# Performance work log

Hardware: AMD Instinct MI355X
Metric: run time of the kernel (lower is better)

The kernel has to match this reference:

```python
import jax, jax.numpy as jnp
import numpy as np

N = 65536   # nodes
E = 1048576 # edges
D_IN = 128
D_H = 64
D_OUT = 2


def setup_inputs() -> dict:
    key = jax.random.key(0)
    ks = jax.random.split(key, 16)
    inp = {
        "x": jax.random.normal(ks[0], (N, D_IN), dtype=jnp.float32),
        "edge_index": jax.random.randint(ks[1], (2, E), 0, N, dtype=jnp.int64),
        "edge_attr": jax.random.uniform(ks[2], (E,), dtype=jnp.float32),
        "W1": jax.random.normal(ks[3], (D_IN, D_H), dtype=jnp.float32) / np.sqrt(D_IN),
        "b1": jnp.zeros((D_H,), dtype=jnp.float32),
        "W2": jax.random.normal(ks[4], (D_H, D_H), dtype=jnp.float32) / np.sqrt(D_H),
        "b2": jnp.zeros((D_H,), dtype=jnp.float32),
        "W3": jax.random.normal(ks[5], (D_H, D_H), dtype=jnp.float32) / np.sqrt(D_H),
        "b3": jnp.zeros((D_H,), dtype=jnp.float32),
        "W4": jax.random.normal(ks[6], (D_H, D_H), dtype=jnp.float32) / np.sqrt(D_H),
        "b4": jnp.zeros((D_H,), dtype=jnp.float32),
        "W5": jax.random.normal(ks[7], (D_H, D_H), dtype=jnp.float32) / np.sqrt(D_H),
        "b5": jnp.zeros((D_H,), dtype=jnp.float32),
        "W8": jax.random.normal(ks[8], (D_H, D_OUT), dtype=jnp.float32) / np.sqrt(D_H),
        "b8": jnp.zeros((D_OUT,), dtype=jnp.float32),
    }
    return inp


def _gcn_layer(x, W, b, row, col, norm):
    # linear transform then degree-normalized scatter-add over edges
    h = x @ W                                              # [N, d_out]
    agg = jax.ops.segment_sum(norm[:, None] * h[row], col, num_segments=N)
    return agg + b


def reference(x, edge_index, edge_attr, W1, b1, W2, b2, W3, b3, W4, b4, W5, b5, W8, b8):
    # gcn_norm with self-loops (PyG GCNConv semantics), shared by all layers
    loop = jnp.arange(N, dtype=edge_index.dtype)
    row = jnp.concatenate([edge_index[0], loop])           # [E+N] sources
    col = jnp.concatenate([edge_index[1], loop])           # [E+N] targets
    ew = jnp.concatenate([edge_attr, jnp.ones((N,), dtype=edge_attr.dtype)])
    deg = jax.ops.segment_sum(ew, col, num_segments=N)     # weighted in-degree
    dinv = jnp.where(deg > 0, deg ** -0.5, 0.0)
    norm = dinv[row] * ew * dinv[col]                      # [E+N]

    h = jax.nn.relu(_gcn_layer(x, W1, b1, row, col, norm))
    h = jax.nn.relu(_gcn_layer(h, W2, b2, row, col, norm))
    # dropout p=0.2 is identity at inference
    h = jax.nn.relu(_gcn_layer(h, W3, b3, row, col, norm))
    h = jax.nn.relu(_gcn_layer(h, W4, b4, row, col, norm))
    h = jax.nn.relu(_gcn_layer(h, W5, b5, row, col, norm))
    return _gcn_layer(h, W8, b8, row, col, norm)           # [N, 2]
```

## Files before the change

### kernel.cpp

```cpp
#include <hip/hip_runtime.h>
#include <hip/hip_bf16.h>
#include <math.h>

#define NN 65536
#define NE 1048576
#define DEG_SCALE 33554432.0f

__device__ inline float4 f4fma(float s, float4 v, float4 a) {
    a.x = fmaf(s, v.x, a.x);
    a.y = fmaf(s, v.y, a.y);
    a.z = fmaf(s, v.z, a.z);
    a.w = fmaf(s, v.w, a.w);
    return a;
}

__device__ inline unsigned pack2bf(float a, float b) {
    __hip_bfloat16 ha = __float2bfloat16(a), hb = __float2bfloat16(b);
    return (unsigned)*reinterpret_cast<unsigned short*>(&ha) |
           ((unsigned)*reinterpret_cast<unsigned short*>(&hb) << 16);
}

__device__ inline void bfx8(uint4 v, float* f) {
    f[0] = __uint_as_float(v.x << 16);
    f[1] = __uint_as_float(v.x & 0xffff0000u);
    f[2] = __uint_as_float(v.y << 16);
    f[3] = __uint_as_float(v.y & 0xffff0000u);
    f[4] = __uint_as_float(v.z << 16);
    f[5] = __uint_as_float(v.z & 0xffff0000u);
    f[6] = __uint_as_float(v.w << 16);
    f[7] = __uint_as_float(v.w & 0xffff0000u);
}

template <int K>
__device__ void mm64_body_bf(const float* __restrict__ A, const float* __restrict__ W,
                             unsigned short* __restrict__ Cb, int node0, int tid) {
    __shared__ float As[64 * 68];
    __shared__ float Ws[64 * 64];
    const int tx = tid & 15;
    const int ty = tid >> 4;
    float4 acc[4];
#pragma unroll
    for (int m = 0; m < 4; ++m) acc[m] = make_float4(0.f, 0.f, 0.f, 0.f);

    for (int kc = 0; kc < K; kc += 64) {
#pragma unroll
        for (int p = 0; p < 4; ++p) {
            int idx = tid + p * 256;
            int r = idx >> 4, c4 = idx & 15;
            float4 v = *reinterpret_cast<const float4*>(A + (size_t)(node0 + r) * K + kc + c4 * 4);
            *reinterpret_cast<float4*>(&As[r * 68 + c4 * 4]) = v;
        }
#pragma unroll
        for (int p = 0; p < 4; ++p) {
            int idx = tid + p * 256;
            int r = idx >> 4, c4 = idx & 15;
            float4 v = *reinterpret_cast<const float4*>(W + (size_t)(kc + r) * 64 + c4 * 4);
            *reinterpret_cast<float4*>(&Ws[r * 64 + c4 * 4]) = v;
        }
        __syncthreads();
#pragma unroll 16
        for (int k = 0; k < 64; ++k) {
            float4 w = *reinterpret_cast<const float4*>(&Ws[k * 64 + tx * 4]);
            float a0 = As[(ty * 4 + 0) * 68 + k];
            float a1 = As[(ty * 4 + 1) * 68 + k];
            float a2 = As[(ty * 4 + 2) * 68 + k];
            float a3 = As[(ty * 4 + 3) * 68 + k];
            acc[0] = f4fma(a0, w, acc[0]);
            acc[1] = f4fma(a1, w, acc[1]);
            acc[2] = f4fma(a2, w, acc[2]);
            acc[3] = f4fma(a3, w, acc[3]);
        }
        __syncthreads();
    }
#pragma unroll
    for (int m = 0; m < 4; ++m) {
        uint2 pk;
        pk.x = pack2bf(acc[m].x, acc[m].y);
        pk.y = pack2bf(acc[m].z, acc[m].w);
        *reinterpret_cast<uint2*>(Cb + (size_t)(node0 + ty * 4 + m) * 64 + tx * 4) = pk;
    }
}


__global__ void __launch_bounds__(256) setup_mm(const int* __restrict__ col,
                                                const float* __restrict__ ew,
                                                unsigned long long* __restrict__ cntdeg,
                                                int* __restrict__ rank,
                                                const float* __restrict__ x,
                                                const float* __restrict__ W1,
                                                unsigned short* __restrict__ Tb) {
    const int bid = blockIdx.x;
    const int tid = threadIdx.x;
    if (bid % 5 == 0) {
        mm64_body_bf<128>(x, W1, Tb, (bid / 5) * 64, tid);
    } else {
        int e = (bid - bid / 5 - 1) * 256 + tid;
        if (e < NE) {
            int c = col[e];
            unsigned long long p =
                (1ull << 32) | (unsigned long long)__float2uint_rn(ew[e] * DEG_SCALE);
            unsigned long long old = atomicAdd(&cntdeg[c], p);
            rank[e] = (int)(old >> 32);
        }
    }
}

__global__ void __launch_bounds__(256) scan1(const unsigned long long* __restrict__ cntdeg,
                                             int* __restrict__ row_ptr,
                                             int* __restrict__ blocksum,
                                             float* __restrict__ dinv) {
    __shared__ int ls[256];
    const int t = threadIdx.x;
    const int i = blockIdx.x * 256 + t;
    unsigned long long v = cntdeg[i];
    const int c = (int)(v >> 32);
    float deg = (float)(unsigned)(v & 0xffffffffull) * (1.0f / DEG_SCALE) + 1.0f;
    dinv[i] = 1.0f / sqrtf(deg);
    ls[t] = c;
    __syncthreads();
#pragma unroll
    for (int off = 1; off < 256; off <<= 1) {
        int u = (t >= off) ? ls[t - off] : 0;
        __syncthreads();
        ls[t] += u;
        __syncthreads();
    }
    row_ptr[i] = ls[t] - c;
    if (t == 255) blocksum[blockIdx.x] = ls[255];
}

__global__ void __launch_bounds__(256) scan2(int* __restrict__ blocksum,
                                             int* __restrict__ blockbase,
                                             int* __restrict__ row_ptr) {
    __shared__ int ls[256];
    const int t = threadIdx.x;
    const int c = blocksum[t];
    ls[t] = c;
    __syncthreads();
#pragma unroll
    for (int off = 1; off < 256; off <<= 1) {
        int u = (t >= off) ? ls[t - off] : 0;
        __syncthreads();
        ls[t] += u;
        __syncthreads();
    }
    blockbase[t] = ls[t] - c;
    if (t == 255) row_ptr[NN] = ls[255];
}

__global__ void __launch_bounds__(256) scan3(int* __restrict__ row_ptr,
                                             const int* __restrict__ blockbase) {
    const int i = blockIdx.x * 256 + threadIdx.x;
    row_ptr[i] += blockbase[blockIdx.x];
}

__global__ void __launch_bounds__(256) fill_kernel(const int* __restrict__ row,
                                                   const int* __restrict__ col,
                                                   const float* __restrict__ ew,
                                                   const float* __restrict__ dinv,
                                                   const int* __restrict__ row_ptr,
                                                   const int* __restrict__ rank,
                                                   int2* __restrict__ epack) {
    int e = blockIdx.x * 256 + threadIdx.x;
    if (e < NE) {
        int c = col[e], r = row[e];
        int idx = row_ptr[c] + rank[e];
        int2 p;
        p.x = r;
        p.y = __float_as_int(dinv[r] * ew[e] * dinv[c]);
        epack[idx] = p;
    }
}


__device__ inline void gather_node(const uint4* __restrict__ T4,
                                   const float* __restrict__ bias,
                                   const float* __restrict__ dinv,
                                   const int* __restrict__ row_ptr,
                                   const int2* __restrict__ epack,
                                   int node, int l, float* acc) {
    const float dv = dinv[node];
    {
        float ts[8];
        bfx8(T4[(size_t)node * 8 + l], ts);
        float4 bA = *reinterpret_cast<const float4*>(bias + l * 8);
        float4 bB = *reinterpret_cast<const float4*>(bias + l * 8 + 4);
        acc[0] = bA.x + dv * dv * ts[0];
        acc[1] = bA.y + dv * dv * ts[1];
        acc[2] = bA.z + dv * dv * ts[2];
        acc[3] = bA.w + dv * dv * ts[3];
        acc[4] = bB.x + dv * dv * ts[4];
        acc[5] = bB.y + dv * dv * ts[5];
        acc[6] = bB.z + dv * dv * ts[6];
        acc[7] = bB.w + dv * dv * ts[7];
    }
    const int s = row_ptr[node];
    const int e = row_ptr[node + 1];
    for (int i0 = s; i0 < e; i0 += 8) {
        int2 p[8];
#pragma unroll
        for (int j = 0; j < 8; ++j) {
            int ii = i0 + j;
            p[j] = epack[ii < e ? ii : i0];
        }
        uint4 r[8];
        float n[8];
#pragma unroll
        for (int j = 0; j < 8; ++j) {
            n[j] = (i0 + j < e) ? __int_as_float(p[j].y) : 0.0f;
            r[j] = T4[(size_t)p[j].x * 8 + l];
        }
#pragma unroll
        for (int j = 0; j < 8; ++j) {
            float f[8];
            bfx8(r[j], f);
#pragma unroll
            for (int k = 0; k < 8; ++k) acc[k] = fmaf(n[j], f[k], acc[k]);
        }
    }
#pragma unroll
    for (int k = 0; k < 8; ++k) acc[k] = fmaxf(acc[k], 0.f);
}

__global__ void __launch_bounds__(256) gmm64(const unsigned short* __restrict__ Tb,
                                             const float* __restrict__ bias,
                                             const float* __restrict__ dinv,
                                             const int* __restrict__ row_ptr,
                                             const int2* __restrict__ epack,
                                             const float* __restrict__ W,
                                             unsigned short* __restrict__ Tbn) {
    __shared__ float As[32 * 68];
    __shared__ float Ws[64 * 64];
    const int tid = threadIdx.x;
    const int node0 = blockIdx.x * 32;

#pragma unroll
    for (int p = 0; p < 4; ++p) {
        int idx = tid + p * 256;
        int r = idx >> 4, c4 = idx & 15;
        *reinterpret_cast<float4*>(&Ws[r * 64 + c4 * 4]) =
            *reinterpret_cast<const float4*>(W + (size_t)r * 64 + c4 * 4);
    }

    const int l = tid & 7;
    const int slot = tid >> 3;
    float acc[8];
    gather_node(reinterpret_cast<const uint4*>(Tb), bias, dinv, row_ptr, epack,
                node0 + slot, l, acc);
    *reinterpret_cast<float4*>(&As[slot * 68 + l * 8]) =
        make_float4(acc[0], acc[1], acc[2], acc[3]);
    *reinterpret_cast<float4*>(&As[slot * 68 + l * 8 + 4]) =
        make_float4(acc[4], acc[5], acc[6], acc[7]);
    __syncthreads();

    const int tx = tid & 15;
    const int ty = tid >> 4;
    float4 c0 = make_float4(0.f, 0.f, 0.f, 0.f);
    float4 c1 = make_float4(0.f, 0.f, 0.f, 0.f);
#pragma unroll 16
    for (int k = 0; k < 64; ++k) {
        float4 w = *reinterpret_cast<const float4*>(&Ws[k * 64 + tx * 4]);
        float a0 = As[(ty * 2 + 0) * 68 + k];
        float a1 = As[(ty * 2 + 1) * 68 + k];
        c0 = f4fma(a0, w, c0);
        c1 = f4fma(a1, w, c1);
    }
    uint2 pk;
    pk.x = pack2bf(c0.x, c0.y);
    pk.y = pack2bf(c0.z, c0.w);
    *reinterpret_cast<uint2*>(Tbn + (size_t)(node0 + ty * 2 + 0) * 64 + tx * 4) = pk;
    pk.x = pack2bf(c1.x, c1.y);
    pk.y = pack2bf(c1.z, c1.w);
    *reinterpret_cast<uint2*>(Tbn + (size_t)(node0 + ty * 2 + 1) * 64 + tx * 4) = pk;
}

__global__ void __launch_bounds__(256) gmm2(const unsigned short* __restrict__ Tb,
                                            const float* __restrict__ bias,
                                            const float* __restrict__ dinv,
                                            const int* __restrict__ row_ptr,
                                            const int2* __restrict__ epack,
                                            const float* __restrict__ W8,
                                            float* __restrict__ T8) {
    __shared__ float As[32 * 68];
    const int tid = threadIdx.x;
    const int node0 = blockIdx.x * 32;
    const int l = tid & 7;
    const int slot = tid >> 3;
    float acc[8];
    gather_node(reinterpret_cast<const uint4*>(Tb), bias, dinv, row_ptr, epack,
                node0 + slot, l, acc);
    *reinterpret_cast<float4*>(&As[slot * 68 + l * 8]) =
        make_float4(acc[0], acc[1], acc[2], acc[3]);
    *reinterpret_cast<float4*>(&As[slot * 68 + l * 8 + 4]) =
        make_float4(acc[4], acc[5], acc[6], acc[7]);
    __syncthreads();
    if (tid < 64) {
        const int nd = tid >> 1, c = tid & 1;
        float s = 0.f;
#pragma unroll 16
        for (int k = 0; k < 64; ++k) s = fmaf(As[nd * 68 + k], W8[k * 2 + c], s);
        T8[(size_t)(node0 + nd) * 2 + c] = s;
    }
}

__global__ void __launch_bounds__(256) gather2(const float* __restrict__ T8,
                                               const float* __restrict__ b8,
                                               const float* __restrict__ dinv,
                                               const int* __restrict__ row_ptr,
                                               const int2* __restrict__ epack,
                                               float* __restrict__ out) {
    const int lane = threadIdx.x & 63;
    const int c = lane & 1;
    const int j = lane >> 1;
    const int node = blockIdx.x * 4 + (threadIdx.x >> 6);
    const int s = row_ptr[node];
    const int e = row_ptr[node + 1];
    float acc = 0.f;
    for (int i = s + j; i < e; i += 32) {
        int2 p = epack[i];
        acc += __int_as_float(p.y) * T8[(size_t)p.x * 2 + c];
    }
    acc += __shfl_xor(acc, 2);
    acc += __shfl_xor(acc, 4);
    acc += __shfl_xor(acc, 8);
    acc += __shfl_xor(acc, 16);
    acc += __shfl_xor(acc, 32);
    if (j == 0) {
        const float dv = dinv[node];
        out[(size_t)node * 2 + c] = b8[c] + dv * dv * T8[(size_t)node * 2 + c] + acc;
    }
}


extern "C" void kernel_launch(void* const* d_in, const int* in_sizes, int n_in,
                              void* d_out, int out_size, void* d_ws, size_t ws_size,
                              hipStream_t stream) {
    const float* x  = (const float*)d_in[0];
    const int*   ei = (const int*)d_in[1];
    const float* ea = (const float*)d_in[2];
    const float* W1 = (const float*)d_in[3];
    const float* b1 = (const float*)d_in[4];
    const float* W2 = (const float*)d_in[5];
    const float* b2 = (const float*)d_in[6];
    const float* W3 = (const float*)d_in[7];
    const float* b3 = (const float*)d_in[8];
    const float* W4 = (const float*)d_in[9];
    const float* b4 = (const float*)d_in[10];
    const float* W5 = (const float*)d_in[11];
    const float* b5 = (const float*)d_in[12];
    const float* W8 = (const float*)d_in[13];
    const float* b8 = (const float*)d_in[14];
    float* out = (float*)d_out;

    unsigned short* Tb1 = (unsigned short*)d_ws;
    unsigned short* Tb2 = Tb1 + (size_t)NN * 64;
    int*   rank   = (int*)Tb2;
    int2*  epack  = (int2*)(Tb2 + (size_t)NN * 64);
    unsigned long long* cntdeg = (unsigned long long*)(epack + NE);
    float* dinv   = (float*)(cntdeg + NN);
    int*   row_ptr= (int*)(dinv + NN);
    float* T8     = (float*)(row_ptr + NN + 1);
    int*   blocksum  = (int*)(T8 + (size_t)NN * 2);
    int*   blockbase = blocksum + 256;

    const int* e_row = ei;
    const int* e_col = ei + NE;

    (void)hipMemsetAsync(cntdeg, 0, (size_t)NN * 8, stream);

    setup_mm<<<5120, 256, 0, stream>>>(e_col, ea, cntdeg, rank, x, W1, Tb1);
    scan1<<<NN / 256, 256, 0, stream>>>(cntdeg, row_ptr, blocksum, dinv);
    scan2<<<1, 256, 0, stream>>>(blocksum, blockbase, row_ptr);
    scan3<<<NN / 256, 256, 0, stream>>>(row_ptr, blockbase);
    fill_kernel<<<NE / 256, 256, 0, stream>>>(e_row, e_col, ea, dinv, row_ptr, rank, epack);

    gmm64<<<NN / 32, 256, 0, stream>>>(Tb1, b1, dinv, row_ptr, epack, W2, Tb2);
    gmm64<<<NN / 32, 256, 0, stream>>>(Tb2, b2, dinv, row_ptr, epack, W3, Tb1);
    gmm64<<<NN / 32, 256, 0, stream>>>(Tb1, b3, dinv, row_ptr, epack, W4, Tb2);
    gmm64<<<NN / 32, 256, 0, stream>>>(Tb2, b4, dinv, row_ptr, epack, W5, Tb1);
    gmm2<<<NN / 32, 256, 0, stream>>>(Tb1, b5, dinv, row_ptr, epack, W8, T8);
    gather2<<<NN / 4, 256, 0, stream>>>(T8, b8, dinv, row_ptr, epack, out);
}
```

Before: 225.7 us.

## Sort nodes by in-degree for balanced gather blocks and store weights as bf16

Builds a degree histogram during the scan, prefix-sums it, and makes a node ordering bucketed by in-degree. The gather+matmul kernels then process nodes in that order, so each block holds nodes of similar degree and lanes sit idle less. Weights and the first-layer input tiles are now stored in shared memory as bf16 to cut LDS footprint and traffic. In exchange there is an extra kernel, an indirect lookup through the order array, scattered output writes, and lower precision for x and W1 in layer one.

Result: slower. 243.8 us (+8.0%).

```diff
diff --git a/kernel.cpp b/kernel.cpp
--- a/kernel.cpp
+++ b/kernel.cpp
@@ -19,6 +19,8 @@
     return (unsigned)*reinterpret_cast<unsigned short*>(&ha) |
            ((unsigned)*reinterpret_cast<unsigned short*>(&hb) << 16);
 }
+
+__device__ inline float bf1(unsigned short u) { return __uint_as_float(((unsigned)u) << 16); }
 
 __device__ inline void bfx8(uint4 v, float* f) {
     f[0] = __uint_as_float(v.x << 16);
@@ -31,40 +33,50 @@
     f[7] = __uint_as_float(v.w & 0xffff0000u);
 }
 
-template <int K>
-__device__ void mm64_body_bf(const float* __restrict__ A, const float* __restrict__ W,
+__device__ void mm64_body_x1(const float* __restrict__ x, const float* __restrict__ W,
                              unsigned short* __restrict__ Cb, int node0, int tid) {
-    __shared__ float As[64 * 68];
-    __shared__ float Ws[64 * 64];
+    __shared__ unsigned short Ash[64 * 72];
+    __shared__ unsigned short Wsh[64 * 64];
     const int tx = tid & 15;
     const int ty = tid >> 4;
     float4 acc[4];
 #pragma unroll
     for (int m = 0; m < 4; ++m) acc[m] = make_float4(0.f, 0.f, 0.f, 0.f);
 
-    for (int kc = 0; kc < K; kc += 64) {
+    for (int kc = 0; kc < 128; kc += 64) {
 #pragma unroll
         for (int p = 0; p < 4; ++p) {
             int idx = tid + p * 256;
             int r = idx >> 4, c4 = idx & 15;
-            float4 v = *reinterpret_cast<const float4*>(A + (size_t)(node0 + r) * K + kc + c4 * 4);
-            *reinterpret_cast<float4*>(&As[r * 68 + c4 * 4]) = v;
+            float4 v = *reinterpret_cast<const float4*>(x + (size_t)(node0 + r) * 128 + kc + c4 * 4);
+            uint2 pk;
+            pk.x = pack2bf(v.x, v.y);
+            pk.y = pack2bf(v.z, v.w);
+            *reinterpret_cast<uint2*>(&Ash[r * 72 + c4 * 4]) = pk;
         }
 #pragma unroll
         for (int p = 0; p < 4; ++p) {
             int idx = tid + p * 256;
             int r = idx >> 4, c4 = idx & 15;
             float4 v = *reinterpret_cast<const float4*>(W + (size_t)(kc + r) * 64 + c4 * 4);
-            *reinterpret_cast<float4*>(&Ws[r * 64 + c4 * 4]) = v;
+            uint2 pk;
+            pk.x = pack2bf(v.x, v.y);
+            pk.y = pack2bf(v.z, v.w);
+            *reinterpret_cast<uint2*>(&Wsh[r * 64 + c4 * 4]) = pk;
         }
         __syncthreads();
 #pragma unroll 16
         for (int k = 0; k < 64; ++k) {
-            float4 w = *reinterpret_cast<const float4*>(&Ws[k * 64 + tx * 4]);
-            float a0 = As[(ty * 4 + 0) * 68 + k];
-            float a1 = As[(ty * 4 + 1) * 68 + k];
-            float a2 = As[(ty * 4 + 2) * 68 + k];
-            float a3 = As[(ty * 4 + 3) * 68 + k];
+            uint2 wp = *reinterpret_cast<uint2*>(&Wsh[k * 64 + tx * 4]);
+            float4 w;
+            w.x = __uint_as_float(wp.x << 16);
+            w.y = __uint_as_float(wp.x & 0xffff0000u);
+            w.z = __uint_as_float(wp.y << 16);
+            w.w = __uint_as_float(wp.y & 0xffff0000u);
+            float a0 = bf1(Ash[(ty * 4 + 0) * 72 + k]);
+            float a1 = bf1(Ash[(ty * 4 + 1) * 72 + k]);
+            float a2 = bf1(Ash[(ty * 4 + 2) * 72 + k]);
+            float a3 = bf1(Ash[(ty * 4 + 3) * 72 + k]);
             acc[0] = f4fma(a0, w, acc[0]);
             acc[1] = f4fma(a1, w, acc[1]);
             acc[2] = f4fma(a2, w, acc[2]);
@@ -92,7 +104,7 @@
     const int bid = blockIdx.x;
     const int tid = threadIdx.x;
     if (bid % 5 == 0) {
-        mm64_body_bf<128>(x, W1, Tb, (bid / 5) * 64, tid);
+        mm64_body_x1(x, W1, Tb, (bid / 5) * 64, tid);
     } else {
         int e = (bid - bid / 5 - 1) * 256 + tid;
         if (e < NE) {
@@ -108,16 +120,22 @@
 __global__ void __launch_bounds__(256) scan1(const unsigned long long* __restrict__ cntdeg,
                                              int* __restrict__ row_ptr,
                                              int* __restrict__ blocksum,
-                                             float* __restrict__ dinv) {
+                                             float* __restrict__ dinv,
+                                             int* __restrict__ deghist) {
     __shared__ int ls[256];
+    __shared__ int hloc[128];
     const int t = threadIdx.x;
     const int i = blockIdx.x * 256 + t;
     unsigned long long v = cntdeg[i];
     const int c = (int)(v >> 32);
     float deg = (float)(unsigned)(v & 0xffffffffull) * (1.0f / DEG_SCALE) + 1.0f;
     dinv[i] = 1.0f / sqrtf(deg);
+    if (t < 128) hloc[t] = 0;
+    __syncthreads();
+    atomicAdd(&hloc[c < 127 ? c : 127], 1);
     ls[t] = c;
     __syncthreads();
+    if (t < 128 && hloc[t] > 0) atomicAdd(&deghist[t], hloc[t]);
 #pragma unroll
     for (int off = 1; off < 256; off <<= 1) {
         int u = (t >= off) ? ls[t - off] : 0;
@@ -129,13 +147,17 @@
     if (t == 255) blocksum[blockIdx.x] = ls[255];
 }
 
-__global__ void __launch_bounds__(256) scan2(int* __restrict__ blocksum,
+__global__ void __launch_bounds__(256) scan2(const int* __restrict__ blocksum,
                                              int* __restrict__ blockbase,
-                                             int* __restrict__ row_ptr) {
+                                             int* __restrict__ row_ptr,
+                                             const int* __restrict__ deghist,
+                                             int* __restrict__ degbase) {
     __shared__ int ls[256];
+    __shared__ int hs[128];
     const int t = threadIdx.x;
     const int c = blocksum[t];
     ls[t] = c;
+    if (t < 128) hs[t] = deghist[t];
     __syncthreads();
 #pragma unroll
     for (int off = 1; off < 256; off <<= 1) {
@@ -146,12 +168,39 @@
     }
     blockbase[t] = ls[t] - c;
     if (t == 255) row_ptr[NN] = ls[255];
+#pragma unroll
+    for (int off = 1; off < 128; off <<= 1) {
+        int u = (t >= off && t < 128) ? hs[t - off] : 0;
+        __syncthreads();
+        if (t < 128) hs[t] += u;
+        __syncthreads();
+    }
+    if (t < 128) degbase[t] = hs[t] - deghist[t];
 }
 
 __global__ void __launch_bounds__(256) scan3(int* __restrict__ row_ptr,
                                              const int* __restrict__ blockbase) {
     const int i = blockIdx.x * 256 + threadIdx.x;
     row_ptr[i] += blockbase[blockIdx.x];
+}
+
+__global__ void __launch_bounds__(256) ord_kernel(const unsigned long long* __restrict__ cntdeg,
+                                                  const int* __restrict__ degbase,
+                                                  int* __restrict__ bincursor,
+                                                  int* __restrict__ order) {
+    __shared__ int hloc[128];
+    __shared__ int base[128];
+    const int t = threadIdx.x;
+    const int i = blockIdx.x * 256 + t;
+    if (t < 128) hloc[t] = 0;
+    __syncthreads();
+    int c = (int)(cntdeg[i] >> 32);
+    if (c > 127) c = 127;
+    int lr = atomicAdd(&hloc[c], 1);
+    __syncthreads();
+    if (t < 128 && hloc[t] > 0) base[t] = atomicAdd(&bincursor[t], hloc[t]);
+    __syncthreads();
+    order[degbase[c] + base[c] + lr] = i;
 }
 
 __global__ void __launch_bounds__(256) fill_kernel(const int* __restrict__ row,
@@ -227,10 +276,11 @@
                                              const float* __restrict__ dinv,
                                              const int* __restrict__ row_ptr,
                                              const int2* __restrict__ epack,
+                                             const int* __restrict__ order,
                                              const float* __restrict__ W,
                                              unsigned short* __restrict__ Tbn) {
     __shared__ float As[32 * 68];
-    __shared__ float Ws[64 * 64];
+    __shared__ unsigned short Wsh[64 * 64];
     const int tid = threadIdx.x;
     const int node0 = blockIdx.x * 32;
 
@@ -238,15 +288,18 @@
     for (int p = 0; p < 4; ++p) {
         int idx = tid + p * 256;
         int r = idx >> 4, c4 = idx & 15;
-        *reinterpret_cast<float4*>(&Ws[r * 64 + c4 * 4]) =
-            *reinterpret_cast<const float4*>(W + (size_t)r * 64 + c4 * 4);
+        float4 v = *reinterpret_cast<const float4*>(W + (size_t)r * 64 + c4 * 4);
+        uint2 pk;
+        pk.x = pack2bf(v.x, v.y);
+        pk.y = pack2bf(v.z, v.w);
+        *reinterpret_cast<uint2*>(&Wsh[r * 64 + c4 * 4]) = pk;
     }
 
     const int l = tid & 7;
     const int slot = tid >> 3;
+    const int node = order[node0 + slot];
     float acc[8];
-    gather_node(reinterpret_cast<const uint4*>(Tb), bias, dinv, row_ptr, epack,
-                node0 + slot, l, acc);
+    gather_node(reinterpret_cast<const uint4*>(Tb), bias, dinv, row_ptr, epack, node, l, acc);
     *reinterpret_cast<float4*>(&As[slot * 68 + l * 8]) =
         make_float4(acc[0], acc[1], acc[2], acc[3]);
     *reinterpret_cast<float4*>(&As[slot * 68 + l * 8 + 4]) =
@@ -259,19 +312,26 @@
     float4 c1 = make_float4(0.f, 0.f, 0.f, 0.f);
 #pragma unroll 16
     for (int k = 0; k < 64; ++k) {
-        float4 w = *reinterpret_cast<const float4*>(&Ws[k * 64 + tx * 4]);
+        uint2 wp = *reinterpret_cast<uint2*>(&Wsh[k * 64 + tx * 4]);
+        float4 w;
+        w.x = __uint_as_float(wp.x << 16);
+        w.y = __uint_as_float(wp.x & 0xffff0000u);
+        w.z = __uint_as_float(wp.y << 16);
+        w.w = __uint_as_float(wp.y & 0xffff0000u);
         float a0 = As[(ty * 2 + 0) * 68 + k];
         float a1 = As[(ty * 2 + 1) * 68 + k];
         c0 = f4fma(a0, w, c0);
         c1 = f4fma(a1, w, c1);
     }
+    const int n0 = order[node0 + ty * 2 + 0];
+    const int n1 = order[node0 + ty * 2 + 1];
     uint2 pk;
     pk.x = pack2bf(c0.x, c0.y);
     pk.y = pack2bf(c0.z, c0.w);
-    *reinterpret_cast<uint2*>(Tbn + (size_t)(node0 + ty * 2 + 0) * 64 + tx * 4) = pk;
+    *reinterpret_cast<uint2*>(Tbn + (size_t)n0 * 64 + tx * 4) = pk;
     pk.x = pack2bf(c1.x, c1.y);
     pk.y = pack2bf(c1.z, c1.w);
-    *reinterpret_cast<uint2*>(Tbn + (size_t)(node0 + ty * 2 + 1) * 64 + tx * 4) = pk;
+    *reinterpret_cast<uint2*>(Tbn + (size_t)n1 * 64 + tx * 4) = pk;
 }
 
 __global__ void __launch_bounds__(256) gmm2(const unsigned short* __restrict__ Tb,
@@ -279,6 +339,7 @@
                                             const float* __restrict__ dinv,
                                             const int* __restrict__ row_ptr,
                                             const int2* __restrict__ epack,
+                                            const int* __restrict__ order,
                                             const float* __restrict__ W8,
                                             float* __restrict__ T8) {
     __shared__ float As[32 * 68];
@@ -286,9 +347,9 @@
     const int node0 = blockIdx.x * 32;
     const int l = tid & 7;
     const int slot = tid >> 3;
+    const int node = order[node0 + slot];
     float acc[8];
-    gather_node(reinterpret_cast<const uint4*>(Tb), bias, dinv, row_ptr, epack,
-                node0 + slot, l, acc);
+    gather_node(reinterpret_cast<const uint4*>(Tb), bias, dinv, row_ptr, epack, node, l, acc);
     *reinterpret_cast<float4*>(&As[slot * 68 + l * 8]) =
         make_float4(acc[0], acc[1], acc[2], acc[3]);
     *reinterpret_cast<float4*>(&As[slot * 68 + l * 8 + 4]) =
@@ -299,7 +360,7 @@
         float s = 0.f;
 #pragma unroll 16
         for (int k = 0; k < 64; ++k) s = fmaf(As[nd * 68 + k], W8[k * 2 + c], s);
-        T8[(size_t)(node0 + nd) * 2 + c] = s;
+        T8[(size_t)order[node0 + nd] * 2 + c] = s;
     }
 }
 
@@ -357,27 +418,32 @@
     int*   rank   = (int*)Tb2;
     int2*  epack  = (int2*)(Tb2 + (size_t)NN * 64);
     unsigned long long* cntdeg = (unsigned long long*)(epack + NE);
-    float* dinv   = (float*)(cntdeg + NN);
+    int*   deghist   = (int*)(cntdeg + NN);
+    int*   bincursor = deghist + 128;
+    int*   degbase   = bincursor + 128;
+    float* dinv   = (float*)(degbase + 128);
     int*   row_ptr= (int*)(dinv + NN);
     float* T8     = (float*)(row_ptr + NN + 1);
     int*   blocksum  = (int*)(T8 + (size_t)NN * 2);
     int*   blockbase = blocksum + 256;
+    int*   order     = blockbase + 256;
 
     const int* e_row = ei;
     const int* e_col = ei + NE;
 
-    (void)hipMemsetAsync(cntdeg, 0, (size_t)NN * 8, stream);
+    (void)hipMemsetAsync(cntdeg, 0, (size_t)NN * 8 + 256 * 4, stream);
 
     setup_mm<<<5120, 256, 0, stream>>>(e_col, ea, cntdeg, rank, x, W1, Tb1);
-    scan1<<<NN / 256, 256, 0, stream>>>(cntdeg, row_ptr, blocksum, dinv);
-    scan2<<<1, 256, 0, stream>>>(blocksum, blockbase, row_ptr);
+    scan1<<<NN / 256, 256, 0, stream>>>(cntdeg, row_ptr, blocksum, dinv, deghist);
+    scan2<<<1, 256, 0, stream>>>(blocksum, blockbase, row_ptr, deghist, degbase);
     scan3<<<NN / 256, 256, 0, stream>>>(row_ptr, blockbase);
+    ord_kernel<<<NN / 256, 256, 0, stream>>>(cntdeg, degbase, bincursor, order);
     fill_kernel<<<NE / 256, 256, 0, stream>>>(e_row, e_col, ea, dinv, row_ptr, rank, epack);
 
-    gmm64<<<NN / 32, 256, 0, stream>>>(Tb1, b1, dinv, row_ptr, epack, W2, Tb2);
-    gmm64<<<NN / 32, 256, 0, stream>>>(Tb2, b2, dinv, row_ptr, epack, W3, Tb1);
-    gmm64<<<NN / 32, 256, 0, stream>>>(Tb1, b3, dinv, row_ptr, epack, W4, Tb2);
-    gmm64<<<NN / 32, 256, 0, stream>>>(Tb2, b4, dinv, row_ptr, epack, W5, Tb1);
-    gmm2<<<NN / 32, 256, 0, stream>>>(Tb1, b5, dinv, row_ptr, epack, W8, T8);
+    gmm64<<<NN / 32, 256, 0, stream>>>(Tb1, b1, dinv, row_ptr, epack, order, W2, Tb2);
+    gmm64<<<NN / 32, 256, 0, stream>>>(Tb2, b2, dinv, row_ptr, epack, order, W3, Tb1);
+    gmm64<<<NN / 32, 256, 0, stream>>>(Tb1, b3, dinv, row_ptr, epack, order, W4, Tb2);
+    gmm64<<<NN / 32, 256, 0, stream>>>(Tb2, b4, dinv, row_ptr, epack, order, W5, Tb1);
+    gmm2<<<NN / 32, 256, 0, stream>>>(Tb1, b5, dinv, row_ptr, epack, order, W8, T8);
     gather2<<<NN / 4, 256, 0, stream>>>(T8, b8, dinv, row_ptr, epack, out);
 }
```
